# Kernel optimization log

Hardware: AMD Instinct MI355X
Metric: run time of the kernel (lower is better)

## Reference

```python
import jax, jax.numpy as jnp
import numpy as np

N, E, C_IN, C_OUT, K = 50000, 800000, 64, 64, 3

def setup_inputs() -> dict:
    key = jax.random.key(0)
    k1, k2, k3, k4, k5, k6 = jax.random.split(key, 6)
    x = jax.random.normal(k1, (N, C_IN), dtype=jnp.float32)
    row = jax.random.randint(k2, (E,), 0, N)
    col = jax.random.randint(k3, (E,), 0, N)
    # PyG ChebConv removes self loops; avoid generating them
    col = jnp.where(col == row, (col + 1) % N, col)
    edge_index = jnp.stack([row, col])
    edge_weight = jax.random.uniform(k4, (E,), dtype=jnp.float32)
    # ChebConv learned params: one [C_in, C_out] matrix per Chebyshev order, plus bias
    W = jax.random.normal(k5, (K, C_IN, C_OUT), dtype=jnp.float32) / np.sqrt(C_IN).astype(np.float32)
    b = jax.random.normal(k6, (C_OUT,), dtype=jnp.float32) * 0.01
    return {"x": x, "edge_index": edge_index, "edge_weight": edge_weight, "W": W, "b": b}


def reference(x, edge_index, edge_weight, W, b):
    row, col = edge_index[0], edge_index[1]
    # PyG ChebConv.__norm__ with sym normalization and lambda_max = 2.0:
    # L_hat = (2/lambda_max) * (I - D^{-1/2} A D^{-1/2}) - I = -D^{-1/2} A D^{-1/2}
    deg = jax.ops.segment_sum(edge_weight, row, num_segments=N)
    dis = jnp.where(deg > 0, jax.lax.rsqrt(deg), 0.0)  # deg_inv_sqrt, inf -> 0
    w = -dis[row] * edge_weight * dis[col]             # [E] normalized Laplacian weights

    def prop(h):  # sparse matvec: L_hat @ h, [N, C]
        return jax.ops.segment_sum(w[:, None] * h[col], row, num_segments=N)

    # Chebyshev recurrence: T0 = x, T1 = L_hat x, Tk = 2 L_hat T_{k-1} - T_{k-2}
    Tx0 = x
    out = Tx0 @ W[0]
    Tx1 = prop(Tx0)
    out = out + Tx1 @ W[1]
    for k in range(2, K):
        Tx2 = 2.0 * prop(Tx1) - Tx0
        out = out + Tx2 @ W[k]
        Tx0, Tx1 = Tx1, Tx2
    return jax.nn.relu(out + b)
```

## Files before the change

### kernel.cpp

```cpp
#include <hip/hip_runtime.h>
#include <hip/hip_bf16.h>

#define C 64
#define NCOPY 8
#define FXSCALE 16777216.0f
#define LOW44 ((1ULL << 44) - 1)

__device__ __forceinline__ unsigned short f2bf_rne(float v) {
    unsigned u = __float_as_uint(v);
    u += 0x7FFFu + ((u >> 16) & 1u);
    return (unsigned short)(u >> 16);
}
__device__ __forceinline__ float bf2f(unsigned short u) {
    return __uint_as_float((unsigned)u << 16);
}

__global__ __launch_bounds__(256) void hist8_kernel(const int* __restrict__ row,
                                                    const float* __restrict__ ew,
                                                    unsigned long long* __restrict__ cd8,
                                                    int* __restrict__ rank,
                                                    int E, int N) {
    int e = blockIdx.x * 256 + threadIdx.x;
    int copy = blockIdx.x & (NCOPY - 1);
    if (e < E) {
        int r = row[e];
        unsigned long long fx = (unsigned long long)__float2uint_rn(ew[e] * FXSCALE);
        unsigned long long inc = (1ULL << 44) | fx;
        unsigned long long old = atomicAdd(&cd8[(size_t)copy * N + r], inc);
        rank[e] = (int)(old >> 44);
    }
}

__global__ __launch_bounds__(256) void cvt_kernel(const float* __restrict__ x,
                                                  unsigned short* __restrict__ xh,
                                                  int total4) {
    int i = blockIdx.x * 256 + threadIdx.x;
    if (i < total4) {
        float4 v = *(const float4*)(x + (size_t)i * 4);
        ushort4 o;
        o.x = f2bf_rne(v.x); o.y = f2bf_rne(v.y);
        o.z = f2bf_rne(v.z); o.w = f2bf_rne(v.w);
        *(ushort4*)(xh + (size_t)i * 4) = o;
    }
}

__global__ __launch_bounds__(256) void scanA_kernel(const unsigned long long* __restrict__ cd8,
                                                    int* __restrict__ cnt,
                                                    float* __restrict__ dis,
                                                    int* __restrict__ bsum, int N) {
    __shared__ int s[256];
    int t = threadIdx.x;
    int i = blockIdx.x * 256 + t;
    int cv = 0;
    unsigned long long dfx = 0;
    if (i < N) {
#pragma unroll
        for (int c = 0; c < NCOPY; c++) {
            unsigned long long v = cd8[(size_t)c * N + i];
            cv += (int)(v >> 44);
            dfx += (v & LOW44);
        }
        cnt[i] = cv;
        float dv = (float)dfx * (1.0f / FXSCALE);
        dis[i] = (dv > 0.0f) ? rsqrtf(dv) : 0.0f;
    }
    s[t] = cv;
    __syncthreads();
    for (int off = 128; off > 0; off >>= 1) {
        if (t < off) s[t] += s[t + off];
        __syncthreads();
    }
    if (t == 0) bsum[blockIdx.x] = s[0];
}

__global__ __launch_bounds__(256) void scanB_kernel(int* __restrict__ bsum,
                                                    int* __restrict__ rowptr,
                                                    int G, int N) {
    __shared__ int s[256];
    int t = threadIdx.x;
    int v = (t < G) ? bsum[t] : 0;
    s[t] = v;
    __syncthreads();
    for (int off = 1; off < 256; off <<= 1) {
        int u = (t >= off) ? s[t - off] : 0;
        __syncthreads();
        s[t] += u;
        __syncthreads();
    }
    if (t < G) bsum[t] = s[t] - v;
    if (t == 255) rowptr[N] = s[255];
}

__global__ __launch_bounds__(256) void scanC_kernel(const int* __restrict__ cnt,
                                                    const unsigned long long* __restrict__ cd8,
                                                    int* __restrict__ start8,
                                                    const int* __restrict__ bsum,
                                                    int* __restrict__ rowptr, int N) {
    __shared__ int s[256];
    int t = threadIdx.x;
    int i = blockIdx.x * 256 + t;
    int v = (i < N) ? cnt[i] : 0;
    s[t] = v;
    __syncthreads();
    for (int off = 1; off < 256; off <<= 1) {
        int u = (t >= off) ? s[t - off] : 0;
        __syncthreads();
        s[t] += u;
        __syncthreads();
    }
    if (i < N) {
        int rp = bsum[blockIdx.x] + s[t] - v;
        rowptr[i] = rp;
        int run = rp;
#pragma unroll
        for (int c = 0; c < NCOPY; c++) {
            int tmp = (int)(cd8[(size_t)c * N + i] >> 44);
            start8[(size_t)c * N + i] = run;
            run += tmp;
        }
    }
}

__global__ __launch_bounds__(256) void scatter_kernel(const int* __restrict__ row,
                                                      const int* __restrict__ col,
                                                      const float* __restrict__ ew,
                                                      const float* __restrict__ dis,
                                                      const int* __restrict__ start8,
                                                      const int* __restrict__ rank,
                                                      float2* __restrict__ ewc,
                                                      int E, int N) {
    int e = blockIdx.x * 256 + threadIdx.x;
    int copy = blockIdx.x & (NCOPY - 1);
    if (e < E) {
        int r = row[e];
        int c = col[e];
        float wv = -dis[r] * ew[e] * dis[c];
        int pos = start8[(size_t)copy * N + r] + rank[e];
        ewc[pos] = make_float2(wv, __int_as_float(c));
    }
}

__global__ __launch_bounds__(256) void spmm_csr_kernel(
        const int* __restrict__ rowptr,
        const float2* __restrict__ ewc,
        const unsigned short* __restrict__ h,
        float* __restrict__ out32,
        unsigned short* __restrict__ outbf,
        int N) {
    int wid = (blockIdx.x * blockDim.x + threadIdx.x) >> 6;
    int lane = threadIdx.x & 63;
    if (wid >= N) return;
    int beg = rowptr[wid];
    int end = rowptr[wid + 1];
    float a0 = 0.0f, a1 = 0.0f, a2 = 0.0f, a3 = 0.0f;
    for (int base = beg; base < end; base += 64) {
        int idx = base + lane;
        float2 ed = (idx < end) ? ewc[idx] : make_float2(0.0f, 0.0f);
        int cnt = end - base; if (cnt > 64) cnt = 64;
        int j = 0;
        for (; j + 3 < cnt; j += 4) {
            float w0 = __int_as_float(__builtin_amdgcn_readlane(__float_as_int(ed.x), j));
            int   c0 = __builtin_amdgcn_readlane(__float_as_int(ed.y), j);
            float w1 = __int_as_float(__builtin_amdgcn_readlane(__float_as_int(ed.x), j + 1));
            int   c1 = __builtin_amdgcn_readlane(__float_as_int(ed.y), j + 1);
            float w2 = __int_as_float(__builtin_amdgcn_readlane(__float_as_int(ed.x), j + 2));
            int   c2 = __builtin_amdgcn_readlane(__float_as_int(ed.y), j + 2);
            float w3 = __int_as_float(__builtin_amdgcn_readlane(__float_as_int(ed.x), j + 3));
            int   c3 = __builtin_amdgcn_readlane(__float_as_int(ed.y), j + 3);
            float h0 = bf2f(h[(size_t)c0 * C + lane]);
            float h1 = bf2f(h[(size_t)c1 * C + lane]);
            float h2 = bf2f(h[(size_t)c2 * C + lane]);
            float h3 = bf2f(h[(size_t)c3 * C + lane]);
            a0 = fmaf(w0, h0, a0);
            a1 = fmaf(w1, h1, a1);
            a2 = fmaf(w2, h2, a2);
            a3 = fmaf(w3, h3, a3);
        }
        for (; j < cnt; j++) {
            float w0 = __int_as_float(__builtin_amdgcn_readlane(__float_as_int(ed.x), j));
            int   c0 = __builtin_amdgcn_readlane(__float_as_int(ed.y), j);
            a0 = fmaf(w0, bf2f(h[(size_t)c0 * C + lane]), a0);
        }
    }
    float acc = (a0 + a1) + (a2 + a3);
    size_t o = (size_t)wid * C + lane;
    out32[o] = acc;
    outbf[o] = f2bf_rne(acc);
}

__global__ __launch_bounds__(256) void final_gemm_kernel(
        const float* __restrict__ x,
        const float* __restrict__ T1,
        const float* __restrict__ P,
        const float* __restrict__ W,
        const float* __restrict__ b,
        float* __restrict__ out, int N) {
    __shared__ float As[16][64];
    __shared__ float Ws[16][64];

    int t  = threadIdx.x;
    int tx = t & 15;
    int ty = t >> 4;
    int n0 = blockIdx.x * 64;

    int sn = t >> 2;
    int skb = (t & 3) * 4;

    float acc[4][4];
#pragma unroll
    for (int i = 0; i < 4; i++)
#pragma unroll
        for (int j = 0; j < 4; j++) acc[i][j] = 0.0f;

#pragma unroll 1
    for (int s = 0; s < 12; s++) {
        float4 wv = *(const float4*)(W + s * 1024 + t * 4);
        int nn = n0 + sn;
        float4 av = make_float4(0.f, 0.f, 0.f, 0.f);
        if (nn < N) {
            if (s < 4) {
                av = *(const float4*)(x + (size_t)nn * C + s * 16 + skb);
            } else if (s < 8) {
                av = *(const float4*)(T1 + (size_t)nn * C + (s - 4) * 16 + skb);
            } else {
                float4 pv = *(const float4*)(P + (size_t)nn * C + (s - 8) * 16 + skb);
                float4 xv = *(const float4*)(x + (size_t)nn * C + (s - 8) * 16 + skb);
                av = make_float4(2.0f * pv.x - xv.x, 2.0f * pv.y - xv.y,
                                 2.0f * pv.z - xv.z, 2.0f * pv.w - xv.w);
            }
        }
        __syncthreads();
        {
            int wk = (t * 4) >> 6;
            int wc = (t * 4) & 63;
            *(float4*)&Ws[wk][wc] = wv;
        }
        As[skb + 0][sn] = av.x;
        As[skb + 1][sn] = av.y;
        As[skb + 2][sn] = av.z;
        As[skb + 3][sn] = av.w;
        __syncthreads();

#pragma unroll
        for (int kk = 0; kk < 16; kk++) {
            float4 a4 = *(const float4*)&As[kk][ty * 4];
            float4 w4 = *(const float4*)&Ws[kk][tx * 4];
            float ar[4] = {a4.x, a4.y, a4.z, a4.w};
            float wr[4] = {w4.x, w4.y, w4.z, w4.w};
#pragma unroll
            for (int i = 0; i < 4; i++)
#pragma unroll
                for (int j = 0; j < 4; j++)
                    acc[i][j] = fmaf(ar[i], wr[j], acc[i][j]);
        }
    }

    float4 bv = *(const float4*)(b + tx * 4);
    float br[4] = {bv.x, bv.y, bv.z, bv.w};
#pragma unroll
    for (int i = 0; i < 4; i++) {
        int node = n0 + ty * 4 + i;
        if (node < N) {
            float4 o;
            o.x = fmaxf(acc[i][0] + br[0], 0.0f);
            o.y = fmaxf(acc[i][1] + br[1], 0.0f);
            o.z = fmaxf(acc[i][2] + br[2], 0.0f);
            o.w = fmaxf(acc[i][3] + br[3], 0.0f);
            *(float4*)(out + (size_t)node * C + tx * 4) = o;
        }
    }
}

extern "C" void kernel_launch(void* const* d_in, const int* in_sizes, int n_in,
                              void* d_out, int out_size, void* d_ws, size_t ws_size,
                              hipStream_t stream) {
    const float* x  = (const float*)d_in[0];
    const int*   ei = (const int*)d_in[1];
    const float* ew = (const float*)d_in[2];
    const float* W  = (const float*)d_in[3];
    const float* b  = (const float*)d_in[4];
    float* out = (float*)d_out;

    const int N = in_sizes[0] / C;
    const int E = in_sizes[2];
    const int* row = ei;
    const int* col = ei + E;

    char* ws = (char*)d_ws;
    size_t off = 0;
    auto alloc = [&](size_t bytes) {
        void* p = ws + off;
        off = (off + bytes + 255) & ~(size_t)255;
        return p;
    };
    float*  dis    = (float*)alloc((size_t)N * 4);
    int*    cnt    = (int*)alloc((size_t)N * 4);
    int*    rowptr = (int*)alloc((size_t)(N + 1) * 4);
    float2* ewc    = (float2*)alloc((size_t)E * 8);
    float*  T1     = (float*)alloc((size_t)N * C * 4);
    float*  P      = (float*)alloc((size_t)N * C * 4);
    int*    bsum   = (int*)alloc((size_t)256 * 4);
    unsigned long long* cd8 = (unsigned long long*)alloc((size_t)NCOPY * N * 8);
    int*    start8 = (int*)alloc((size_t)NCOPY * N * 4);
    int*    rank   = (int*)alloc((size_t)E * 4);
    unsigned short* xh  = (unsigned short*)alloc((size_t)N * C * 2);
    unsigned short* T1h = (unsigned short*)alloc((size_t)N * C * 2);
    unsigned short* Ph  = (unsigned short*)alloc((size_t)N * C * 2);

    hipMemsetAsync(cd8, 0, (size_t)NCOPY * N * 8, stream);

    const int B = 256;
    const int G = (N + B - 1) / B;

    hist8_kernel<<<(E + B - 1) / B, B, 0, stream>>>(row, ew, cd8, rank, E, N);
    int total4 = N * C / 4;
    cvt_kernel<<<(total4 + B - 1) / B, B, 0, stream>>>(x, xh, total4);
    scanA_kernel<<<G, B, 0, stream>>>(cd8, cnt, dis, bsum, N);
    scanB_kernel<<<1, B, 0, stream>>>(bsum, rowptr, G, N);
    scanC_kernel<<<G, B, 0, stream>>>(cnt, cd8, start8, bsum, rowptr, N);
    scatter_kernel<<<(E + B - 1) / B, B, 0, stream>>>(row, col, ew, dis, start8,
                                                      rank, ewc, E, N);

    int spmm_blocks = (int)(((long long)N * 64 + B - 1) / B);
    spmm_csr_kernel<<<spmm_blocks, B, 0, stream>>>(rowptr, ewc, xh, T1, T1h, N);
    spmm_csr_kernel<<<spmm_blocks, B, 0, stream>>>(rowptr, ewc, T1h, P, Ph, N);

    final_gemm_kernel<<<(N + 63) / 64, B, 0, stream>>>(x, T1, P, W, b, out, N);
}
```

Before: 213.8 us.

## Replace global atomic CSR build with LDS-histogram chunked sort and factor out degree scaling

Result: slower. 294.6 us (+37.8%).

```diff
diff --git a/kernel.cpp b/kernel.cpp
--- a/kernel.cpp
+++ b/kernel.cpp
@@ -2,69 +2,77 @@
 #include <hip/hip_bf16.h>
 
 #define C 64
-#define NCOPY 8
-#define FXSCALE 16777216.0f
-#define LOW44 ((1ULL << 44) - 1)
-
-__device__ __forceinline__ unsigned short f2bf_rne(float v) {
+#define KCH 128
+#define RPP 12500
+
+typedef unsigned short u16;
+
+__device__ __forceinline__ u16 f2bf_rne(float v) {
     unsigned u = __float_as_uint(v);
     u += 0x7FFFu + ((u >> 16) & 1u);
-    return (unsigned short)(u >> 16);
-}
-__device__ __forceinline__ float bf2f(unsigned short u) {
+    return (u16)(u >> 16);
+}
+__device__ __forceinline__ float bf2f(u16 u) {
     return __uint_as_float((unsigned)u << 16);
 }
 
-__global__ __launch_bounds__(256) void hist8_kernel(const int* __restrict__ row,
-                                                    const float* __restrict__ ew,
-                                                    unsigned long long* __restrict__ cd8,
-                                                    int* __restrict__ rank,
-                                                    int E, int N) {
-    int e = blockIdx.x * 256 + threadIdx.x;
-    int copy = blockIdx.x & (NCOPY - 1);
-    if (e < E) {
-        int r = row[e];
-        unsigned long long fx = (unsigned long long)__float2uint_rn(ew[e] * FXSCALE);
-        unsigned long long inc = (1ULL << 44) | fx;
-        unsigned long long old = atomicAdd(&cd8[(size_t)copy * N + r], inc);
-        rank[e] = (int)(old >> 44);
-    }
-}
-
-__global__ __launch_bounds__(256) void cvt_kernel(const float* __restrict__ x,
-                                                  unsigned short* __restrict__ xh,
-                                                  int total4) {
-    int i = blockIdx.x * 256 + threadIdx.x;
-    if (i < total4) {
-        float4 v = *(const float4*)(x + (size_t)i * 4);
-        ushort4 o;
-        o.x = f2bf_rne(v.x); o.y = f2bf_rne(v.y);
-        o.z = f2bf_rne(v.z); o.w = f2bf_rne(v.w);
-        *(ushort4*)(xh + (size_t)i * 4) = o;
-    }
-}
-
-__global__ __launch_bounds__(256) void scanA_kernel(const unsigned long long* __restrict__ cd8,
-                                                    int* __restrict__ cnt,
-                                                    float* __restrict__ dis,
-                                                    int* __restrict__ bsum, int N) {
+__global__ __launch_bounds__(256) void hist_kernel(const int* __restrict__ row,
+                                                   u16* __restrict__ cnt16,
+                                                   u16* __restrict__ rank16,
+                                                   int E, int N, int chunk) {
+    __shared__ unsigned lcnt[RPP];
+    int k = blockIdx.x;
+    int t = threadIdx.x;
+    int ebeg = k * chunk;
+    int eend = min(E, ebeg + chunk);
+    int passes = (N + RPP - 1) / RPP;
+    for (int p = 0; p < passes; p++) {
+        int rbase = p * RPP;
+        int rcount = min(RPP, N - rbase);
+        for (int i = t; i < rcount; i += 256) lcnt[i] = 0;
+        __syncthreads();
+        for (int e = ebeg + t; e < eend; e += 256) {
+            unsigned rr = (unsigned)(row[e] - rbase);
+            if (rr < (unsigned)rcount) {
+                unsigned old = atomicAdd(&lcnt[rr], 1u);
+                rank16[e] = (u16)old;
+            }
+        }
+        __syncthreads();
+        unsigned* dst = (unsigned*)(cnt16 + (size_t)k * N + rbase);
+        int pairs = rcount >> 1;
+        for (int i = t; i < pairs; i += 256)
+            dst[i] = (lcnt[2 * i] & 0xffffu) | (lcnt[2 * i + 1] << 16);
+        if ((rcount & 1) && t == 0)
+            cnt16[(size_t)k * N + rbase + rcount - 1] = (u16)lcnt[rcount - 1];
+        __syncthreads();
+    }
+}
+
+__global__ __launch_bounds__(256) void scanA_kernel(const u16* __restrict__ cnt16,
+                                                    int* __restrict__ cnttot,
+                                                    int* __restrict__ bsum,
+                                                    int N, int K) {
     __shared__ int s[256];
     int t = threadIdx.x;
-    int i = blockIdx.x * 256 + t;
-    int cv = 0;
-    unsigned long long dfx = 0;
-    if (i < N) {
-#pragma unroll
-        for (int c = 0; c < NCOPY; c++) {
-            unsigned long long v = cd8[(size_t)c * N + i];
-            cv += (int)(v >> 44);
-            dfx += (v & LOW44);
-        }
-        cnt[i] = cv;
-        float dv = (float)dfx * (1.0f / FXSCALE);
-        dis[i] = (dv > 0.0f) ? rsqrtf(dv) : 0.0f;
-    }
-    s[t] = cv;
+    int base = blockIdx.x * 512;
+    int r0 = base + 2 * t, r1 = r0 + 1;
+    int tot0 = 0, tot1 = 0;
+    for (int k = 0; k < K; k++) {
+        if (r0 < N) {
+            size_t o = (size_t)k * N + r0;
+            if (r1 < N) {
+                unsigned v = *(const unsigned*)(cnt16 + o);
+                tot0 += (int)(v & 0xffffu);
+                tot1 += (int)(v >> 16);
+            } else {
+                tot0 += (int)cnt16[o];
+            }
+        }
+    }
+    if (r0 < N) cnttot[r0] = tot0;
+    if (r1 < N) cnttot[r1] = tot1;
+    s[t] = tot0 + tot1;
     __syncthreads();
     for (int off = 128; off > 0; off >>= 1) {
         if (t < off) s[t] += s[t + off];
@@ -91,16 +99,20 @@
     if (t == 255) rowptr[N] = s[255];
 }
 
-__global__ __launch_bounds__(256) void scanC_kernel(const int* __restrict__ cnt,
-                                                    const unsigned long long* __restrict__ cd8,
-                                                    int* __restrict__ start8,
+__global__ __launch_bounds__(256) void scanC_kernel(const u16* __restrict__ cnt16,
+                                                    const int* __restrict__ cnttot,
                                                     const int* __restrict__ bsum,
-                                                    int* __restrict__ rowptr, int N) {
+                                                    int* __restrict__ rowptr,
+                                                    unsigned* __restrict__ prefix32,
+                                                    int N, int K) {
     __shared__ int s[256];
     int t = threadIdx.x;
-    int i = blockIdx.x * 256 + t;
-    int v = (i < N) ? cnt[i] : 0;
-    s[t] = v;
+    int base = blockIdx.x * 512;
+    int r0 = base + 2 * t, r1 = r0 + 1;
+    int v0 = (r0 < N) ? cnttot[r0] : 0;
+    int v1 = (r1 < N) ? cnttot[r1] : 0;
+    int pair = v0 + v1;
+    s[t] = pair;
     __syncthreads();
     for (int off = 1; off < 256; off <<= 1) {
         int u = (t >= off) ? s[t - off] : 0;
@@ -108,15 +120,25 @@
         s[t] += u;
         __syncthreads();
     }
-    if (i < N) {
-        int rp = bsum[blockIdx.x] + s[t] - v;
-        rowptr[i] = rp;
-        int run = rp;
-#pragma unroll
-        for (int c = 0; c < NCOPY; c++) {
-            int tmp = (int)(cd8[(size_t)c * N + i] >> 44);
-            start8[(size_t)c * N + i] = run;
-            run += tmp;
+    int ex = bsum[blockIdx.x] + s[t] - pair;
+    int rp0 = ex, rp1 = ex + v0;
+    if (r0 < N) rowptr[r0] = rp0;
+    if (r1 < N) rowptr[r1] = rp1;
+    unsigned run0 = (unsigned)rp0, run1 = (unsigned)rp1;
+    for (int k = 0; k < K; k++) {
+        size_t o = (size_t)k * N + r0;
+        if (r0 < N) {
+            if (r1 < N) {
+                unsigned v = *(const unsigned*)(cnt16 + o);
+                uint2 pr; pr.x = run0; pr.y = run1;
+                *(uint2*)(prefix32 + o) = pr;
+                run0 += (v & 0xffffu);
+                run1 += (v >> 16);
+            } else {
+                unsigned v = cnt16[o];
+                prefix32[o] = run0;
+                run0 += v;
+            }
         }
     }
 }
@@ -124,29 +146,75 @@
 __global__ __launch_bounds__(256) void scatter_kernel(const int* __restrict__ row,
                                                       const int* __restrict__ col,
                                                       const float* __restrict__ ew,
-                                                      const float* __restrict__ dis,
-                                                      const int* __restrict__ start8,
-                                                      const int* __restrict__ rank,
+                                                      const u16* __restrict__ rank16,
+                                                      const unsigned* __restrict__ prefix32,
                                                       float2* __restrict__ ewc,
-                                                      int E, int N) {
-    int e = blockIdx.x * 256 + threadIdx.x;
-    int copy = blockIdx.x & (NCOPY - 1);
-    if (e < E) {
-        int r = row[e];
-        int c = col[e];
-        float wv = -dis[r] * ew[e] * dis[c];
-        int pos = start8[(size_t)copy * N + r] + rank[e];
-        ewc[pos] = make_float2(wv, __int_as_float(c));
+                                                      int E, int N, int chunk) {
+    int k = blockIdx.x;
+    int t = threadIdx.x;
+    int ebeg = k * chunk;
+    int eend = min(E, ebeg + chunk);
+    size_t kb = (size_t)k * N;
+    for (int g = ebeg; g < eend; g += 1024) {
+        int e[4]; unsigned pos[4]; int cc[4]; float wv[4];
+#pragma unroll
+        for (int u = 0; u < 4; u++) {
+            e[u] = g + u * 256 + t;
+            if (e[u] < eend) {
+                int r = row[e[u]];
+                pos[u] = prefix32[kb + r] + rank16[e[u]];
+                cc[u] = col[e[u]];
+                wv[u] = ew[e[u]];
+            }
+        }
+#pragma unroll
+        for (int u = 0; u < 4; u++)
+            if (e[u] < eend) ewc[pos[u]] = make_float2(wv[u], __int_as_float(cc[u]));
+    }
+}
+
+__global__ __launch_bounds__(256) void degdis_kernel(const int* __restrict__ rowptr,
+                                                     const float2* __restrict__ ewc,
+                                                     const float* __restrict__ x,
+                                                     float* __restrict__ dis,
+                                                     u16* __restrict__ g,
+                                                     int N) {
+    __shared__ float sdis[256];
+    int t = threadIdx.x;
+    int r = blockIdx.x * 256 + t;
+    if (r < N) {
+        int b = rowptr[r], en = rowptr[r + 1];
+        float dv = 0.0f;
+        for (int p = b; p < en; p++) dv += ewc[p].x;
+        float di = (dv > 0.0f) ? rsqrtf(dv) : 0.0f;
+        dis[r] = di;
+        sdis[t] = di;
+    }
+    __syncthreads();
+    size_t nb = (size_t)blockIdx.x * 16384;
+    for (int i = 0; i < 16; i++) {
+        int idx4 = i * 256 + t;
+        int lr = idx4 >> 4;
+        int gr = blockIdx.x * 256 + lr;
+        if (gr < N) {
+            float4 v = *(const float4*)(x + nb + (size_t)idx4 * 4);
+            float di = sdis[lr];
+            ushort4 o;
+            o.x = f2bf_rne(v.x * di); o.y = f2bf_rne(v.y * di);
+            o.z = f2bf_rne(v.z * di); o.w = f2bf_rne(v.w * di);
+            *(ushort4*)(g + nb + (size_t)idx4 * 4) = o;
+        }
     }
 }
 
 __global__ __launch_bounds__(256) void spmm_csr_kernel(
         const int* __restrict__ rowptr,
         const float2* __restrict__ ewc,
-        const unsigned short* __restrict__ h,
+        const float* __restrict__ dis,
+        const u16* __restrict__ h,
         float* __restrict__ out32,
-        unsigned short* __restrict__ outbf,
-        int N) {
+        u16* __restrict__ outbf,
+        int N, int writebf) {
     int wid = (blockIdx.x * blockDim.x + threadIdx.x) >> 6;
     int lane = threadIdx.x & 63;
     if (wid >= N) return;
@@ -182,10 +250,11 @@
             a0 = fmaf(w0, bf2f(h[(size_t)c0 * C + lane]), a0);
         }
     }
-    float acc = (a0 + a1) + (a2 + a3);
+    float dr = dis[wid];
+    float res = -dr * ((a0 + a1) + (a2 + a3));
     size_t o = (size_t)wid * C + lane;
-    out32[o] = acc;
-    outbf[o] = f2bf_rne(acc);
+    out32[o] = res;
+    if (writebf) outbf[o] = f2bf_rne(dr * res);
 }
 
 __global__ __launch_bounds__(256) void final_gemm_kernel(
@@ -293,37 +362,34 @@
         off = (off + bytes + 255) & ~(size_t)255;
         return p;
     };
-    float*  dis    = (float*)alloc((size_t)N * 4);
-    int*    cnt    = (int*)alloc((size_t)N * 4);
-    int*    rowptr = (int*)alloc((size_t)(N + 1) * 4);
-    float2* ewc    = (float2*)alloc((size_t)E * 8);
-    float*  T1     = (float*)alloc((size_t)N * C * 4);
-    float*  P      = (float*)alloc((size_t)N * C * 4);
-    int*    bsum   = (int*)alloc((size_t)256 * 4);
-    unsigned long long* cd8 = (unsigned long long*)alloc((size_t)NCOPY * N * 8);
-    int*    start8 = (int*)alloc((size_t)NCOPY * N * 4);
-    int*    rank   = (int*)alloc((size_t)E * 4);
-    unsigned short* xh  = (unsigned short*)alloc((size_t)N * C * 2);
-    unsigned short* T1h = (unsigned short*)alloc((size_t)N * C * 2);
-    unsigned short* Ph  = (unsigned short*)alloc((size_t)N * C * 2);
-
-    hipMemsetAsync(cd8, 0, (size_t)NCOPY * N * 8, stream);
+    float*    dis      = (float*)alloc((size_t)N * 4);
+    int*      cnttot   = (int*)alloc((size_t)N * 4);
+    int*      rowptr   = (int*)alloc((size_t)(N + 1) * 4);
+    float2*   ewc      = (float2*)alloc((size_t)E * 8);
+    float*    T1       = (float*)alloc((size_t)N * C * 4);
+    float*    P        = (float*)alloc((size_t)N * C * 4);
+    int*      bsum     = (int*)alloc((size_t)256 * 4);
+    u16*      cnt16    = (u16*)alloc((size_t)KCH * N * 2);
+    unsigned* prefix32 = (unsigned*)alloc((size_t)KCH * N * 4);
+    u16*      rank16   = (u16*)alloc((size_t)E * 2);
+    u16*      xg       = (u16*)alloc((size_t)N * C * 2);
+    u16*      T1g      = (u16*)alloc((size_t)N * C * 2);
 
     const int B = 256;
-    const int G = (N + B - 1) / B;
-
-    hist8_kernel<<<(E + B - 1) / B, B, 0, stream>>>(row, ew, cd8, rank, E, N);
-    int total4 = N * C / 4;
-    cvt_kernel<<<(total4 + B - 1) / B, B, 0, stream>>>(x, xh, total4);
-    scanA_kernel<<<G, B, 0, stream>>>(cd8, cnt, dis, bsum, N);
-    scanB_kernel<<<1, B, 0, stream>>>(bsum, rowptr, G, N);
-    scanC_kernel<<<G, B, 0, stream>>>(cnt, cd8, start8, bsum, rowptr, N);
-    scatter_kernel<<<(E + B - 1) / B, B, 0, stream>>>(row, col, ew, dis, start8,
-                                                      rank, ewc, E, N);
+    const int chunk = (E + KCH - 1) / KCH;
+    const int G2 = (N + 511) / 512;
+
+    hist_kernel<<<KCH, B, 0, stream>>>(row, cnt16, rank16, E, N, chunk);
+    scanA_kernel<<<G2, B, 0, stream>>>(cnt16, cnttot, bsum, N, KCH);
+    scanB_kernel<<<1, B, 0, stream>>>(bsum, rowptr, G2, N);
+    scanC_kernel<<<G2, B, 0, stream>>>(cnt16, cnttot, bsum, rowptr, prefix32, N, KCH);
+    scatter_kernel<<<KCH, B, 0, stream>>>(row, col, ew, rank16, prefix32, ewc,
+                                          E, N, chunk);
+    degdis_kernel<<<(N + 255) / 256, B, 0, stream>>>(rowptr, ewc, x, dis, xg, N);
 
     int spmm_blocks = (int)(((long long)N * 64 + B - 1) / B);
-    spmm_csr_kernel<<<spmm_blocks, B, 0, stream>>>(rowptr, ewc, xh, T1, T1h, N);
-    spmm_csr_kernel<<<spmm_blocks, B, 0, stream>>>(rowptr, ewc, T1h, P, Ph, N);
+    spmm_csr_kernel<<<spmm_blocks, B, 0, stream>>>(rowptr, ewc, dis, xg, T1, T1g, N, 1);
+    spmm_csr_kernel<<<spmm_blocks, B, 0, stream>>>(rowptr, ewc, dis, T1g, P, T1g, N, 0);
 
     final_gemm_kernel<<<(N + 63) / 64, B, 0, stream>>>(x, T1, P, W, b, out, N);
 }
```
